# Optimization experiments

Hardware: AMD Instinct MI355X
Metric: run time of the kernel (lower is better)

Reference implementation:

```python
import jax, jax.numpy as jnp
import numpy as np

B, L, D, H = 8, 1500, 1024, 8
HD = D // H
N_BOUNDARIES = 300  # exactly 300 boundaries per sequence -> max_segments = 300
EPS = 1e-5


def setup_inputs() -> dict:
    key = jax.random.key(0)
    ks = jax.random.split(key, 6)
    rng = np.random.default_rng(0)
    boundaries = np.zeros((B, L), dtype=np.float32)
    for b in range(B):
        boundaries[b, rng.permutation(L)[:N_BOUNDARIES]] = 1.0
    lengths = rng.uniform(0.5, 1.0, size=(B,)).astype(np.float32)
    hidden = jax.random.normal(ks[0], (B, L, D), jnp.float32)
    learned_query = jax.random.normal(ks[1], (D,), jnp.float32) * 0.02
    eye = jnp.eye(D, dtype=jnp.float32)
    # identity-initialized projections, perturbed so the test is non-trivial
    Wk = eye + 0.02 * jax.random.normal(ks[2], (D, D), jnp.float32)
    Wv = eye + 0.02 * jax.random.normal(ks[3], (D, D), jnp.float32)
    Wo = eye + 0.02 * jax.random.normal(ks[4], (D, D), jnp.float32)
    return {
        'hidden': hidden,
        'boundaries': jnp.asarray(boundaries),
        'lengths': jnp.asarray(lengths),
        'learned_query': learned_query,
        'Wk': Wk, 'Wv': Wv, 'Wo': Wo,
        'ln_gamma': jnp.ones((D,), jnp.float32),
        'ln_beta': jnp.zeros((D,), jnp.float32),
        'max_segments': N_BOUNDARIES,
    }


def _attention_pooling(hidden, boundaries, lengths, learned_query, Wk, Wv, Wo,
                       ln_gamma, ln_beta, max_segments):
    # segment id per token: cumsum(b) - b (token before first boundary -> seg 0)
    seg_id = jnp.cumsum(boundaries, axis=1) - boundaries            # (B, L)
    # foo[b,t,s] = s - seg_id[b,t]; foo == 0 -> token t belongs to segment s
    seg_mask = (jnp.arange(max_segments)[None, None, :] == seg_id[:, :, None])
    actual_lens = (lengths * L).astype(jnp.int32)                   # (B,)
    len_mask = jnp.arange(L)[None, :] < actual_lens[:, None]        # (B, L)
    seg_mask = seg_mask & len_mask[:, :, None]                      # (B, L, S) bool

    # LayerNorm (biased variance, as torch.nn.LayerNorm)
    mu = jnp.mean(hidden, axis=-1, keepdims=True)
    var = jnp.var(hidden, axis=-1, keepdims=True)
    hn = (hidden - mu) * jax.lax.rsqrt(var + EPS) * ln_gamma + ln_beta

    k = (hn @ Wk.T).reshape(B, L, H, HD)
    v = (hn @ Wv.T).reshape(B, L, H, HD)
    q = learned_query.reshape(H, HD)
    # queries are the same learned vector for every segment -> compute (B,H,L)
    # once and broadcast across S (same math as the original dense matmul)
    scores = jnp.einsum('hd,blhd->bhl', q, k) * (HD ** -0.5)        # (B, H, L)

    mask = seg_mask.transpose(0, 2, 1)[:, None, :, :]               # (B, 1, S, L)
    scores4 = jnp.where(mask, scores[:, :, None, :], -1e30)         # (B, H, S, L)
    w = jax.nn.softmax(scores4, axis=-1)
    w = jnp.where(mask, w, 0.0)
    # rows with no valid token: softmax of all -inf -> nan_to_num(0) in torch
    row_valid = jnp.any(mask, axis=-1, keepdims=True)
    w = jnp.where(row_valid, w, 0.0)

    pooled = jnp.einsum('bhsl,blhd->bshd', w, v).reshape(B, max_segments, D)
    return pooled @ Wo.T                                            # (B, S, D)


def reference(hidden, boundaries, lengths, learned_query, Wk, Wv, Wo,
              ln_gamma, ln_beta, max_segments):
    return _attention_pooling(hidden, boundaries, lengths, learned_query,
                              Wk, Wv, Wo, ln_gamma, ln_beta, max_segments)
```

## Files before the change

kernel.cpp:

```cpp
#include <hip/hip_runtime.h>
#include <hip/hip_bf16.h>

#define BPK_B 8
#define BPK_L 1500
#define BPK_D 1024
#define BPK_H 8
#define BPK_S 300
#define BPK_EPS 1e-5f
#define BPK_M (BPK_B * BPK_L)
#define BPK_MS (BPK_B * BPK_S)
#define BPK_MS_TILES 19
#define BPK_HP_ROWS 2432
#define BPK_PO_PAD 3072

typedef __hip_bfloat16 bf16;
typedef __bf16 bf16x8 __attribute__((ext_vector_type(8)));
typedef float v4f __attribute__((ext_vector_type(4)));

static __device__ __forceinline__ float bf_lo(unsigned u) {
    return __uint_as_float((u & 0xffffu) << 16);
}
static __device__ __forceinline__ float bf_hi(unsigned u) {
    return __uint_as_float((u >> 16) << 16);
}
static __device__ __forceinline__ void bpk_store(float v, float* p) { *p = v; }
static __device__ __forceinline__ void bpk_store(float v, bf16* p) { *p = __float2bfloat16(v); }
static __device__ __forceinline__ uint2 pack4bf(float a, float b, float c, float d) {
    union { bf16 h[4]; uint2 u; } pk;
    pk.h[0] = __float2bfloat16(a); pk.h[1] = __float2bfloat16(b);
    pk.h[2] = __float2bfloat16(c); pk.h[3] = __float2bfloat16(d);
    return pk.u;
}

#define BPK_GL2LDS(gsrc, ldst)                                                 \
    __builtin_amdgcn_global_load_lds(                                          \
        (const __attribute__((address_space(1))) void*)(gsrc),                 \
        (__attribute__((address_space(3))) void*)(ldst), 16, 0, 0)

__global__ __launch_bounds__(256) void bpk_prep_kernel(
    const float* __restrict__ Wv, const float* __restrict__ Wo,
    const float* __restrict__ lq, const float* __restrict__ Wk,
    const float* __restrict__ boundaries, const float* __restrict__ lengths,
    bf16* __restrict__ wvb, bf16* __restrict__ wob, bf16* __restrict__ qkb,
    int* __restrict__ seg_start, int* __restrict__ seg_cnt) {
    __shared__ unsigned char flags[1536];
    __shared__ int st_sh[BPK_S + 2];
    __shared__ int wsumi[4];
    int blk = blockIdx.x;
    int tid = threadIdx.x;
    if (blk < 2048) {
        const float* s = blk < 1024 ? Wv : Wo;
        bf16* d = blk < 1024 ? wvb : wob;
        int i = ((blk & 1023) * 256 + tid) * 4;
        float4 v = *(const float4*)(s + i);
        *(uint2*)(d + i) = pack4bf(v.x, v.y, v.z, v.w);
        return;
    }
    if (blk < 2080) {
        int o = (blk - 2048) * 256 + tid;
        int h = o >> 10, k = o & 1023;
        const float* wr = Wk + (size_t)(h * 128) * BPK_D + k;
        const float* qr = lq + h * 128;
        float s = 0.f;
        #pragma unroll 8
        for (int d = 0; d < 128; d++)
            s += qr[d] * wr[(size_t)d * BPK_D];
        qkb[o] = __float2bfloat16(s);
        return;
    }
    int b = blk - 2080;
    int alen = (int)(lengths[b] * (float)BPK_L);
    const float* bd = boundaries + (size_t)b * BPK_L;
    for (int t = tid; t < 1536; t += 256)
        flags[t] = (t < BPK_L && bd[t] >= 0.5f) ? 1 : 0;
    for (int s = tid; s < BPK_S + 2; s += 256) st_sh[s] = BPK_L;
    __syncthreads();
    int base = tid * 6;
    int lsum = 0;
    #pragma unroll
    for (int j = 0; j < 6; j++) lsum += flags[base + j];
    int lane = tid & 63, wid = tid >> 6;
    int scan = lsum;
    #pragma unroll
    for (int off = 1; off < 64; off <<= 1) {
        int u = __shfl_up(scan, off);
        if (lane >= off) scan += u;
    }
    if (lane == 63) wsumi[wid] = scan;
    __syncthreads();
    int wbase = 0;
    for (int w = 0; w < wid; w++) wbase += wsumi[w];
    int run = wbase + scan - lsum;
    #pragma unroll
    for (int j = 0; j < 6; j++) {
        int t = base + j;
        if (t < BPK_L) {
            int sid = run;
            if ((t == 0 || flags[t - 1]) && sid <= BPK_S) st_sh[sid] = t;
            if (flags[t]) run++;
        }
    }
    __syncthreads();
    for (int s = tid; s < BPK_S; s += 256) {
        int st = st_sh[s];
        int e = min(st_sh[s + 1], alen);
        int s0 = min(st, alen);
        seg_start[b * BPK_S + s] = st;
        seg_cnt[b * BPK_S + s] = max(0, e - s0);
    }
}

__global__ __launch_bounds__(256) void bpk_ln_score_kernel(
    const float* __restrict__ x, const float* __restrict__ gamma,
    const float* __restrict__ beta, const bf16* __restrict__ qkb,
    const float* __restrict__ lengths,
    float2* __restrict__ murs, float* __restrict__ scores) {
    int tid = threadIdx.x;
    int lane = tid & 63, wid = tid >> 6;
    float4 g[4], bb[4];
    uint2 qk[8][4];
    #pragma unroll
    for (int j = 0; j < 4; j++) {
        g[j]  = *(const float4*)(gamma + j * 256 + lane * 4);
        bb[j] = *(const float4*)(beta + j * 256 + lane * 4);
    }
    #pragma unroll
    for (int h = 0; h < 8; h++)
        #pragma unroll
        for (int j = 0; j < 4; j++)
            qk[h][j] = *(const uint2*)(qkb + h * BPK_D + j * 256 + lane * 4);
    float lv = (lane < BPK_B) ? lengths[lane] : 0.f;
    const bool b0 = (lane & 1) != 0;
    const bool b1 = (lane & 2) != 0;
    const bool b2 = (lane & 4) != 0;
    const int head = 4 * (lane & 1) + (lane & 2) + ((lane >> 2) & 1);

    const int nwaves = gridDim.x * 4;
    for (int row = blockIdx.x * 4 + wid; row < BPK_M; row += nwaves) {
        int b = row / BPK_L, t = row - b * BPK_L;
        float alenf = __shfl(lv, b);
        if (t >= (int)(alenf * (float)BPK_L)) continue;
        const float* xr = x + (size_t)row * BPK_D;
        float4 f[4];
        float s = 0.f, sq = 0.f;
        #pragma unroll
        for (int j = 0; j < 4; j++) {
            f[j] = *(const float4*)(xr + j * 256 + lane * 4);
            s  += f[j].x + f[j].y + f[j].z + f[j].w;
            sq += f[j].x * f[j].x + f[j].y * f[j].y
                + f[j].z * f[j].z + f[j].w * f[j].w;
        }
        #pragma unroll
        for (int off = 1; off < 64; off <<= 1) {
            s  += __shfl_xor(s, off);
            sq += __shfl_xor(sq, off);
        }
        float mu = s * (1.0f / BPK_D);
        float var = sq * (1.0f / BPK_D) - mu * mu;
        float rs = rsqrtf(var + BPK_EPS);
        float p[8];
        #pragma unroll
        for (int h = 0; h < 8; h++) p[h] = 0.f;
        #pragma unroll
        for (int j = 0; j < 4; j++) {
            float h0 = (f[j].x - mu) * rs * g[j].x + bb[j].x;
            float h1 = (f[j].y - mu) * rs * g[j].y + bb[j].y;
            float h2 = (f[j].z - mu) * rs * g[j].z + bb[j].z;
            float h3 = (f[j].w - mu) * rs * g[j].w + bb[j].w;
            #pragma unroll
            for (int h = 0; h < 8; h++) {
                uint2 qv = qk[h][j];
                p[h] += h0 * bf_lo(qv.x) + h1 * bf_hi(qv.x)
                      + h2 * bf_lo(qv.y) + h3 * bf_hi(qv.y);
            }
        }
        #pragma unroll
        for (int r = 0; r < 4; r++) {
            float send = b0 ? p[r] : p[r + 4];
            float recv = __shfl_xor(send, 1);
            p[r]     += b0 ? 0.f : recv;
            p[r + 4] += b0 ? recv : 0.f;
        }
        float q0 = b0 ? p[4] : p[0];
        float q1 = b0 ? p[5] : p[1];
        float q2 = b0 ? p[6] : p[2];
        float q3 = b0 ? p[7] : p[3];
        {
            float send = b1 ? q0 : q2;
            float recv = __shfl_xor(send, 2);
            q0 += b1 ? 0.f : recv;
            q2 += b1 ? recv : 0.f;
            send = b1 ? q1 : q3;
            recv = __shfl_xor(send, 2);
            q1 += b1 ? 0.f : recv;
            q3 += b1 ? recv : 0.f;
        }
        float a = b1 ? q2 : q0;
        float c = b1 ? q3 : q1;
        float send = b2 ? a : c;
        float recv = __shfl_xor(send, 4);
        float v = (b2 ? c : a) + recv;
        v += __shfl_xor(v, 8);
        v += __shfl_xor(v, 16);
        v += __shfl_xor(v, 32);
        if (lane < 8) {
            scores[((size_t)b * BPK_H + head) * BPK_L + t] =
                v * 0.088388347648318447f;
        } else if (lane == 8) {
            murs[row] = make_float2(mu, rs);
        }
    }
}

__global__ __launch_bounds__(256) void bpk_pool_kernel(
    const float* __restrict__ scores, const float* __restrict__ x,
    const float* __restrict__ gamma, const float* __restrict__ beta,
    const float2* __restrict__ murs,
    const int* __restrict__ seg_start, const int* __restrict__ seg_cnt,
    bf16* __restrict__ hpool) {
    int bs = blockIdx.x;
    int b = bs / BPK_S;
    int tid = threadIdx.x;
    int lane = tid & 63, wid = tid >> 6;
    __shared__ float minv[8][2];
    __shared__ float wls[8][128];
    int cnt = seg_cnt[bs], st = seg_start[bs];
    float4 g4 = *(const float4*)(gamma + tid * 4);
    float4 b4 = *(const float4*)(beta + tid * 4);
    float acc[8][4];
    #pragma unroll
    for (int h = 0; h < 8; h++)
        #pragma unroll
        for (int j = 0; j < 4; j++) acc[h][j] = 0.f;
    if (cnt > 0) {
        if (wid == 0) {
            int h = lane & 7, i0 = lane >> 3;
            const float* sc = scores + ((size_t)(b * 8 + h)) * BPK_L + st;
            float m = -1e30f;
            for (int i = i0; i < cnt; i += 8) m = fmaxf(m, sc[i]);
            #pragma unroll
            for (int off = 8; off < 64; off <<= 1) m = fmaxf(m, __shfl_xor(m, off));
            float l = 0.f;
            for (int i = i0; i < cnt; i += 8) l += __expf(sc[i] - m);
            #pragma unroll
            for (int off = 8; off < 64; off <<= 1) l += __shfl_xor(l, off);
            if (i0 == 0) { minv[h][0] = m; minv[h][1] = 1.0f / l; }
        }
        __syncthreads();
        for (int cb = 0; cb < cnt; cb += 128) {
            int cc = min(128, cnt - cb);
            int hh = tid >> 5, i0 = (tid & 31) * 4;
            #pragma unroll
            for (int j = 0; j < 4; j++) {
                int i = i0 + j;
                if (i < cc)
                    wls[hh][i] = __expf(scores[((size_t)(b * 8 + hh)) * BPK_L + st + cb + i]
                                        - minv[hh][0]) * minv[hh][1];
            }
            __syncthreads();
            const float* xp = x + (size_t)(b * BPK_L + st + cb) * BPK_D + tid * 4;
            const float2* mp = murs + (size_t)(b * BPK_L + st + cb);
            for (int i = 0; i < cc; i++) {
                float4 f = *(const float4*)(xp + (size_t)i * BPK_D);
                float2 mr = mp[i];
                float x0 = (f.x - mr.x) * mr.y * g4.x + b4.x;
                float x1 = (f.y - mr.x) * mr.y * g4.y + b4.y;
                float x2 = (f.z - mr.x) * mr.y * g4.z + b4.z;
                float x3 = (f.w - mr.x) * mr.y * g4.w + b4.w;
                #pragma unroll
                for (int h = 0; h < 8; h++) {
                    float w = wls[h][i];
                    acc[h][0] += w * x0; acc[h][1] += w * x1;
                    acc[h][2] += w * x2; acc[h][3] += w * x3;
                }
            }
            __syncthreads();
        }
    }
    #pragma unroll
    for (int h = 0; h < 8; h++)
        *(uint2*)(hpool + ((size_t)h * BPK_HP_ROWS + bs) * BPK_D + tid * 4) =
            pack4bf(acc[h][0], acc[h][1], acc[h][2], acc[h][3]);
}

__global__ __launch_bounds__(256) void bpk_headgemm_kernel(
    const bf16* __restrict__ hpool, const bf16* __restrict__ wvb,
    bf16* __restrict__ pooled) {
    const int mt = blockIdx.x, h = blockIdx.y;
    const int m0 = mt * 128;
    const bf16* A = hpool + (size_t)h * BPK_HP_ROWS * BPK_D;
    const bf16* W = wvb + (size_t)(h * 128) * BPK_D;
    __shared__ bf16 As[128][32];
    __shared__ bf16 Bs[128][32];
    const int tid = threadIdx.x;
    const int lane = tid & 63, wid = tid >> 6;
    const int wm = (wid & 1) * 64, wn = (wid >> 1) * 64;
    const int lm = lane & 15, quad = lane >> 4;
    const int c0 = wid * 2;
    const int rA = c0 * 16 + (lane >> 2);
    const int colc = (lane & 3) * 8;

    v4f acc[4][4];
    #pragma unroll
    for (int i = 0; i < 4; i++)
        #pragma unroll
        for (int j = 0; j < 4; j++) acc[i][j] = (v4f){0.f, 0.f, 0.f, 0.f};

    for (int k0 = 0; k0 < BPK_D; k0 += 32) {
        const bf16* pa = &A[(size_t)(m0 + rA) * BPK_D + k0 + colc];
        const bf16* pw = &W[(size_t)rA * BPK_D + k0 + colc];
        BPK_GL2LDS(pa, &As[c0 * 16][0]);
        BPK_GL2LDS(pa + (size_t)16 * BPK_D, &As[(c0 + 1) * 16][0]);
        BPK_GL2LDS(pw, &Bs[c0 * 16][0]);
        BPK_GL2LDS(pw + (size_t)16 * BPK_D, &Bs[(c0 + 1) * 16][0]);
        __syncthreads();
        bf16x8 af[4], bfr[4];
        #pragma unroll
        for (int i = 0; i < 4; i++)
            af[i] = *(const bf16x8*)&As[wm + i * 16 + lm][quad * 8];
        #pragma unroll
        for (int j = 0; j < 4; j++)
            bfr[j] = *(const bf16x8*)&Bs[wn + j * 16 + lm][quad * 8];
        #pragma unroll
        for (int i = 0; i < 4; i++)
            #pragma unroll
            for (int j = 0; j < 4; j++)
                acc[i][j] = __builtin_amdgcn_mfma_f32_16x16x32_bf16(af[i], bfr[j], acc[i][j], 0, 0, 0);
        __syncthreads();
    }
    #pragma unroll
    for (int i = 0; i < 4; i++) {
        int mbase = m0 + wm + i * 16 + quad * 4;
        #pragma unroll
        for (int j = 0; j < 4; j++) {
            int col = h * 128 + wn + j * 16 + lm;
            #pragma unroll
            for (int r = 0; r < 4; r++) {
                int m = mbase + r;
                if (m < BPK_MS)
                    pooled[(size_t)m * BPK_D + col] = __float2bfloat16(acc[i][j][r]);
            }
        }
    }
}

template <typename OT>
__global__ __launch_bounds__(256) void bpk_gemm_bt_kernel(
    const bf16* __restrict__ A, const bf16* __restrict__ W,
    OT* __restrict__ O, int M, int NT) {
    const int flat = blockIdx.x;
    const int xcd = flat & 7, slot = flat >> 3;
    const int mt = xcd + 8 * (slot / NT);
    const int nt = slot % NT;
    const int n0 = nt * 128;
    const int m0 = mt * 128;
    __shared__ bf16 As[128][32];
    __shared__ bf16 Bs[128][32];
    const int tid = threadIdx.x;
    const int lane = tid & 63, wid = tid >> 6;
    const int wm = (wid & 1) * 64, wn = (wid >> 1) * 64;
    const int lm = lane & 15, quad = lane >> 4;
    const int c0 = wid * 2;
    const int rA = c0 * 16 + (lane >> 2);
    const int colc = (lane & 3) * 8;

    v4f acc[4][4];
    #pragma unroll
    for (int i = 0; i < 4; i++)
        #pragma unroll
        for (int j = 0; j < 4; j++) acc[i][j] = (v4f){0.f, 0.f, 0.f, 0.f};

    for (int k0 = 0; k0 < BPK_D; k0 += 32) {
        const bf16* pa = &A[(size_t)(m0 + rA) * BPK_D + k0 + colc];
        const bf16* pw = &W[(size_t)(n0 + rA) * BPK_D + k0 + colc];
        BPK_GL2LDS(pa, &As[c0 * 16][0]);
        BPK_GL2LDS(pa + (size_t)16 * BPK_D, &As[(c0 + 1) * 16][0]);
        BPK_GL2LDS(pw, &Bs[c0 * 16][0]);
        BPK_GL2LDS(pw + (size_t)16 * BPK_D, &Bs[(c0 + 1) * 16][0]);
        __syncthreads();
        bf16x8 af[4], bfr[4];
        #pragma unroll
        for (int i = 0; i < 4; i++)
            af[i] = *(const bf16x8*)&As[wm + i * 16 + lm][quad * 8];
        #pragma unroll
        for (int j = 0; j < 4; j++)
            bfr[j] = *(const bf16x8*)&Bs[wn + j * 16 + lm][quad * 8];
        #pragma unroll
        for (int i = 0; i < 4; i++)
            #pragma unroll
            for (int j = 0; j < 4; j++)
                acc[i][j] = __builtin_amdgcn_mfma_f32_16x16x32_bf16(af[i], bfr[j], acc[i][j], 0, 0, 0);
        __syncthreads();
    }
    #pragma unroll
    for (int i = 0; i < 4; i++) {
        int mbase = m0 + wm + i * 16 + quad * 4;
        #pragma unroll
        for (int j = 0; j < 4; j++) {
            int col = n0 + wn + j * 16 + lm;
            #pragma unroll
            for (int r = 0; r < 4; r++) {
                int m = mbase + r;
                if (m < M) bpk_store(acc[i][j][r], &O[(size_t)m * BPK_D + col]);
            }
        }
    }
}

extern "C" void kernel_launch(void* const* d_in, const int* in_sizes, int n_in,
                              void* d_out, int out_size, void* d_ws, size_t ws_size,
                              hipStream_t stream) {
    const float* hidden     = (const float*)d_in[0];
    const float* boundaries = (const float*)d_in[1];
    const float* lengths    = (const float*)d_in[2];
    const float* lq         = (const float*)d_in[3];
    const float* Wk         = (const float*)d_in[4];
    const float* Wv         = (const float*)d_in[5];
    const float* Wo         = (const float*)d_in[6];
    const float* gamma      = (const float*)d_in[7];
    const float* beta       = (const float*)d_in[8];
    float* out              = (float*)d_out;

    char* ws = (char*)d_ws;
    size_t off = 0;
    auto carve = [&](size_t bytes) -> char* {
        char* p = ws + off;
        off += (bytes + 255) & ~(size_t)255;
        return p;
    };
    bf16* hpool    = (bf16*)carve((size_t)BPK_H * BPK_HP_ROWS * BPK_D * sizeof(bf16));
    bf16* pooled   = (bf16*)carve((size_t)BPK_PO_PAD * BPK_D * sizeof(bf16));
    bf16* wvb      = (bf16*)carve((size_t)BPK_D * BPK_D * sizeof(bf16));
    bf16* wob      = (bf16*)carve((size_t)BPK_D * BPK_D * sizeof(bf16));
    bf16* qkb      = (bf16*)carve((size_t)BPK_H * BPK_D * sizeof(bf16));
    float* scores  = (float*)carve((size_t)BPK_B * BPK_H * BPK_L * sizeof(float));
    float2* murs   = (float2*)carve((size_t)BPK_M * sizeof(float2));
    int* seg_start = (int*)carve((size_t)BPK_B * BPK_S * sizeof(int));
    int* seg_cnt   = (int*)carve((size_t)BPK_B * BPK_S * sizeof(int));

    bpk_prep_kernel<<<dim3(2088), dim3(256), 0, stream>>>(
        Wv, Wo, lq, Wk, boundaries, lengths, wvb, wob, qkb, seg_start, seg_cnt);
    bpk_ln_score_kernel<<<dim3(1024), dim3(256), 0, stream>>>(
        hidden, gamma, beta, qkb, lengths, murs, scores);
    bpk_pool_kernel<<<dim3(BPK_MS), dim3(256), 0, stream>>>(
        scores, hidden, gamma, beta, murs, seg_start, seg_cnt, hpool);
    bpk_headgemm_kernel<<<dim3(BPK_MS_TILES, BPK_H), dim3(256), 0, stream>>>(
        hpool, wvb, pooled);
    bpk_gemm_bt_kernel<float><<<dim3((BPK_PO_PAD / 128) * 8), dim3(256), 0, stream>>>(
        pooled, wob, out, BPK_MS, 8);
}
```

Baseline: 191.7 us.

## Shrink GEMM tiles to 64x64 and move weight conversion into LN kernel

Both GEMMs (per-head value GEMM and output projection) switch from 128x128 to 64x64 block tiles. This multiplies the number of workgroups so the small M=2400 problems can fill more compute units. The Wv/Wo fp32-to-bf16 conversion moves from the prep kernel into extra blocks of the LayerNorm/score kernel. That shrinks the prep kernel to 40 blocks and lets the conversion run alongside the LN work. The trade-off is less data reuse per tile and more LDS loads per MFMA.

```diff
diff --git a/kernel.cpp b/kernel.cpp
--- a/kernel.cpp
+++ b/kernel.cpp
@@ -9,9 +9,8 @@
 #define BPK_EPS 1e-5f
 #define BPK_M (BPK_B * BPK_L)
 #define BPK_MS (BPK_B * BPK_S)
-#define BPK_MS_TILES 19
 #define BPK_HP_ROWS 2432
-#define BPK_PO_PAD 3072
+#define BPK_PO_PAD 2560
 
 typedef __hip_bfloat16 bf16;
 typedef __bf16 bf16x8 __attribute__((ext_vector_type(8)));
@@ -38,26 +37,16 @@
         (__attribute__((address_space(3))) void*)(ldst), 16, 0, 0)
 
 __global__ __launch_bounds__(256) void bpk_prep_kernel(
-    const float* __restrict__ Wv, const float* __restrict__ Wo,
     const float* __restrict__ lq, const float* __restrict__ Wk,
     const float* __restrict__ boundaries, const float* __restrict__ lengths,
-    bf16* __restrict__ wvb, bf16* __restrict__ wob, bf16* __restrict__ qkb,
-    int* __restrict__ seg_start, int* __restrict__ seg_cnt) {
+    bf16* __restrict__ qkb, int* __restrict__ seg_start, int* __restrict__ seg_cnt) {
     __shared__ unsigned char flags[1536];
     __shared__ int st_sh[BPK_S + 2];
     __shared__ int wsumi[4];
     int blk = blockIdx.x;
     int tid = threadIdx.x;
-    if (blk < 2048) {
-        const float* s = blk < 1024 ? Wv : Wo;
-        bf16* d = blk < 1024 ? wvb : wob;
-        int i = ((blk & 1023) * 256 + tid) * 4;
-        float4 v = *(const float4*)(s + i);
-        *(uint2*)(d + i) = pack4bf(v.x, v.y, v.z, v.w);
-        return;
-    }
-    if (blk < 2080) {
-        int o = (blk - 2048) * 256 + tid;
+    if (blk < 32) {
+        int o = blk * 256 + tid;
         int h = o >> 10, k = o & 1023;
         const float* wr = Wk + (size_t)(h * 128) * BPK_D + k;
         const float* qr = lq + h * 128;
@@ -68,7 +57,7 @@
         qkb[o] = __float2bfloat16(s);
         return;
     }
-    int b = blk - 2080;
+    int b = blk - 32;
     int alen = (int)(lengths[b] * (float)BPK_L);
     const float* bd = boundaries + (size_t)b * BPK_L;
     for (int t = tid; t < 1536; t += 256)
@@ -110,12 +99,23 @@
     }
 }
 
-__global__ __launch_bounds__(256) void bpk_ln_score_kernel(
+__global__ __launch_bounds__(256) void bpk_ln_score_conv_kernel(
     const float* __restrict__ x, const float* __restrict__ gamma,
     const float* __restrict__ beta, const bf16* __restrict__ qkb,
     const float* __restrict__ lengths,
+    const float* __restrict__ Wv, const float* __restrict__ Wo,
+    bf16* __restrict__ wvb, bf16* __restrict__ wob,
     float2* __restrict__ murs, float* __restrict__ scores) {
     int tid = threadIdx.x;
+    if (blockIdx.x >= 1024) {
+        int cb = blockIdx.x - 1024;
+        const float* s = cb < 1024 ? Wv : Wo;
+        bf16* d = cb < 1024 ? wvb : wob;
+        int i = ((cb & 1023) * 256 + tid) * 4;
+        float4 v = *(const float4*)(s + i);
+        *(uint2*)(d + i) = pack4bf(v.x, v.y, v.z, v.w);
+        return;
+    }
     int lane = tid & 63, wid = tid >> 6;
     float4 g[4], bb[4];
     uint2 qk[8][4];
@@ -135,7 +135,7 @@
     const bool b2 = (lane & 4) != 0;
     const int head = 4 * (lane & 1) + (lane & 2) + ((lane >> 2) & 1);
 
-    const int nwaves = gridDim.x * 4;
+    const int nwaves = 1024 * 4;
     for (int row = blockIdx.x * 4 + wid; row < BPK_M; row += nwaves) {
         int b = row / BPK_L, t = row - b * BPK_L;
         float alenf = __shfl(lv, b);
@@ -286,54 +286,49 @@
 __global__ __launch_bounds__(256) void bpk_headgemm_kernel(
     const bf16* __restrict__ hpool, const bf16* __restrict__ wvb,
     bf16* __restrict__ pooled) {
-    const int mt = blockIdx.x, h = blockIdx.y;
-    const int m0 = mt * 128;
+    const int mt = blockIdx.x >> 1, nt = blockIdx.x & 1, h = blockIdx.y;
+    const int m0 = mt * 64, n0 = nt * 64;
     const bf16* A = hpool + (size_t)h * BPK_HP_ROWS * BPK_D;
-    const bf16* W = wvb + (size_t)(h * 128) * BPK_D;
-    __shared__ bf16 As[128][32];
-    __shared__ bf16 Bs[128][32];
+    const bf16* W = wvb + (size_t)(h * 128 + n0) * BPK_D;
+    __shared__ bf16 As[64][32];
+    __shared__ bf16 Bs[64][32];
     const int tid = threadIdx.x;
     const int lane = tid & 63, wid = tid >> 6;
-    const int wm = (wid & 1) * 64, wn = (wid >> 1) * 64;
+    const int wm = (wid & 1) * 32, wn = (wid >> 1) * 32;
     const int lm = lane & 15, quad = lane >> 4;
-    const int c0 = wid * 2;
-    const int rA = c0 * 16 + (lane >> 2);
+    const int rA = wid * 16 + (lane >> 2);
     const int colc = (lane & 3) * 8;
 
-    v4f acc[4][4];
-    #pragma unroll
-    for (int i = 0; i < 4; i++)
-        #pragma unroll
-        for (int j = 0; j < 4; j++) acc[i][j] = (v4f){0.f, 0.f, 0.f, 0.f};
+    v4f acc[2][2];
+    #pragma unroll
+    for (int i = 0; i < 2; i++)
+        #pragma unroll
+        for (int j = 0; j < 2; j++) acc[i][j] = (v4f){0.f, 0.f, 0.f, 0.f};
 
     for (int k0 = 0; k0 < BPK_D; k0 += 32) {
-        const bf16* pa = &A[(size_t)(m0 + rA) * BPK_D + k0 + colc];
-        const bf16* pw = &W[(size_t)rA * BPK_D + k0 + colc];
-        BPK_GL2LDS(pa, &As[c0 * 16][0]);
-        BPK_GL2LDS(pa + (size_t)16 * BPK_D, &As[(c0 + 1) * 16][0]);
-        BPK_GL2LDS(pw, &Bs[c0 * 16][0]);
-        BPK_GL2LDS(pw + (size_t)16 * BPK_D, &Bs[(c0 + 1) * 16][0]);
+        BPK_GL2LDS(&A[(size_t)(m0 + rA) * BPK_D + k0 + colc], &As[wid * 16][0]);
+        BPK_GL2LDS(&W[(size_t)rA * BPK_D + k0 + colc], &Bs[wid * 16][0]);
         __syncthreads();
-        bf16x8 af[4], bfr[4];
-        #pragma unroll
-        for (int i = 0; i < 4; i++)
+        bf16x8 af[2], bfr[2];
+        #pragma unroll
+        for (int i = 0; i < 2; i++)
             af[i] = *(const bf16x8*)&As[wm + i * 16 + lm][quad * 8];
         #pragma unroll
-        for (int j = 0; j < 4; j++)
+        for (int j = 0; j < 2; j++)
             bfr[j] = *(const bf16x8*)&Bs[wn + j * 16 + lm][quad * 8];
         #pragma unroll
-        for (int i = 0; i < 4; i++)
-            #pragma unroll
-            for (int j = 0; j < 4; j++)
+        for (int i = 0; i < 2; i++)
+            #pragma unroll
+            for (int j = 0; j < 2; j++)
                 acc[i][j] = __builtin_amdgcn_mfma_f32_16x16x32_bf16(af[i], bfr[j], acc[i][j], 0, 0, 0);
         __syncthreads();
     }
     #pragma unroll
-    for (int i = 0; i < 4; i++) {
+    for (int i = 0; i < 2; i++) {
         int mbase = m0 + wm + i * 16 + quad * 4;
         #pragma unroll
-        for (int j = 0; j < 4; j++) {
-            int col = h * 128 + wn + j * 16 + lm;
+        for (int j = 0; j < 2; j++) {
+            int col = h * 128 + n0 + wn + j * 16 + lm;
             #pragma unroll
             for (int r = 0; r < 4; r++) {
                 int m = mbase + r;
@@ -344,64 +339,57 @@
     }
 }
 
-template <typename OT>
-__global__ __launch_bounds__(256) void bpk_gemm_bt_kernel(
+__global__ __launch_bounds__(256) void bpk_ogemm_kernel(
     const bf16* __restrict__ A, const bf16* __restrict__ W,
-    OT* __restrict__ O, int M, int NT) {
+    float* __restrict__ O) {
     const int flat = blockIdx.x;
     const int xcd = flat & 7, slot = flat >> 3;
-    const int mt = xcd + 8 * (slot / NT);
-    const int nt = slot % NT;
-    const int n0 = nt * 128;
-    const int m0 = mt * 128;
-    __shared__ bf16 As[128][32];
-    __shared__ bf16 Bs[128][32];
+    const int mt = xcd + 8 * (slot >> 4);
+    const int nt = slot & 15;
+    const int m0 = mt * 64, n0 = nt * 64;
+    __shared__ bf16 As[64][32];
+    __shared__ bf16 Bs[64][32];
     const int tid = threadIdx.x;
     const int lane = tid & 63, wid = tid >> 6;
-    const int wm = (wid & 1) * 64, wn = (wid >> 1) * 64;
+    const int wm = (wid & 1) * 32, wn = (wid >> 1) * 32;
     const int lm = lane & 15, quad = lane >> 4;
-    const int c0 = wid * 2;
-    const int rA = c0 * 16 + (lane >> 2);
+    const int rA = wid * 16 + (lane >> 2);
     const int colc = (lane & 3) * 8;
 
-    v4f acc[4][4];
-    #pragma unroll
-    for (int i = 0; i < 4; i++)
-        #pragma unroll
-        for (int j = 0; j < 4; j++) acc[i][j] = (v4f){0.f, 0.f, 0.f, 0.f};
+    v4f acc[2][2];
+    #pragma unroll
+    for (int i = 0; i < 2; i++)
+        #pragma unroll
+        for (int j = 0; j < 2; j++) acc[i][j] = (v4f){0.f, 0.f, 0.f, 0.f};
 
     for (int k0 = 0; k0 < BPK_D; k0 += 32) {
-        const bf16* pa = &A[(size_t)(m0 + rA) * BPK_D + k0 + colc];
-        const bf16* pw = &W[(size_t)(n0 + rA) * BPK_D + k0 + colc];
-        BPK_GL2LDS(pa, &As[c0 * 16][0]);
-        BPK_GL2LDS(pa + (size_t)16 * BPK_D, &As[(c0 + 1) * 16][0]);
-        BPK_GL2LDS(pw, &Bs[c0 * 16][0]);
-        BPK_GL2LDS(pw + (size_t)16 * BPK_D, &Bs[(c0 + 1) * 16][0]);
+        BPK_GL2LDS(&A[(size_t)(m0 + rA) * BPK_D + k0 + colc], &As[wid * 16][0]);
+        BPK_GL2LDS(&W[(size_t)(n0 + rA) * BPK_D + k0 + colc], &Bs[wid * 16][0]);
         __syncthreads();
-        bf16x8 af[4], bfr[4];
-        #pragma unroll
-        for (int i = 0; i < 4; i++)
+        bf16x8 af[2], bfr[2];
+        #pragma unroll
+        for (int i = 0; i < 2; i++)
             af[i] = *(const bf16x8*)&As[wm + i * 16 + lm][quad * 8];
         #pragma unroll
-        for (int j = 0; j < 4; j++)
+        for (int j = 0; j < 2; j++)
             bfr[j] = *(const bf16x8*)&Bs[wn + j * 16 + lm][quad * 8];
         #pragma unroll
-        for (int i = 0; i < 4; i++)
-            #pragma unroll
-            for (int j = 0; j < 4; j++)
+        for (int i = 0; i < 2; i++)
+            #pragma unroll
+            for (int j = 0; j < 2; j++)
                 acc[i][j] = __builtin_amdgcn_mfma_f32_16x16x32_bf16(af[i], bfr[j], acc[i][j], 0, 0, 0);
         __syncthreads();
     }
     #pragma unroll
-    for (int i = 0; i < 4; i++) {
+    for (int i = 0; i < 2; i++) {
         int mbase = m0 + wm + i * 16 + quad * 4;
         #pragma unroll
-        for (int j = 0; j < 4; j++) {
+        for (int j = 0; j < 2; j++) {
             int col = n0 + wn + j * 16 + lm;
             #pragma unroll
             for (int r = 0; r < 4; r++) {
                 int m = mbase + r;
-                if (m < M) bpk_store(acc[i][j][r], &O[(size_t)m * BPK_D + col]);
+                if (m < BPK_MS) O[(size_t)m * BPK_D + col] = acc[i][j][r];
             }
         }
     }
@@ -438,14 +426,14 @@
     int* seg_start = (int*)carve((size_t)BPK_B * BPK_S * sizeof(int));
     int* seg_cnt   = (int*)carve((size_t)BPK_B * BPK_S * sizeof(int));
 
-    bpk_prep_kernel<<<dim3(2088), dim3(256), 0, stream>>>(
-        Wv, Wo, lq, Wk, boundaries, lengths, wvb, wob, qkb, seg_start, seg_cnt);
-    bpk_ln_score_kernel<<<dim3(1024), dim3(256), 0, stream>>>(
-        hidden, gamma, beta, qkb, lengths, murs, scores);
+    bpk_prep_kernel<<<dim3(40), dim3(256), 0, stream>>>(
+        lq, Wk, boundaries, lengths, qkb, seg_start, seg_cnt);
+    bpk_ln_score_conv_kernel<<<dim3(3072), dim3(256), 0, stream>>>(
+        hidden, gamma, beta, qkb, lengths, Wv, Wo, wvb, wob, murs, scores);
     bpk_pool_kernel<<<dim3(BPK_MS), dim3(256), 0, stream>>>(
         scores, hidden, gamma, beta, murs, seg_start, seg_cnt, hpool);
-    bpk_headgemm_kernel<<<dim3(BPK_MS_TILES, BPK_H), dim3(256), 0, stream>>>(
+    bpk_headgemm_kernel<<<dim3(76, BPK_H), dim3(256), 0, stream>>>(
         hpool, wvb, pooled);
-    bpk_gemm_bt_kernel<float><<<dim3((BPK_PO_PAD / 128) * 8), dim3(256), 0, stream>>>(
-        pooled, wob, out, BPK_MS, 8);
-}
+    bpk_ogemm_kernel<<<dim3(640), dim3(256), 0, stream>>>(
+        pooled, wob, out);
+}
```

Measured after the change: 173.9 us. 9.3% less time.
